# Kernel optimization log

Hardware: AMD Instinct MI355X
Metric: run time of the kernel (lower is better)

Reference implementation:

```python
import jax, jax.numpy as jnp
import numpy as np

N_NODES = 100000
N_EDGES = 1600000
IN_F, HID_F, OUT_F = 64, 64, 64


def setup_inputs() -> dict:
    key = jax.random.key(0)
    ks = jax.random.split(key, 9)
    return {
        "x": jax.random.normal(ks[0], (N_NODES, IN_F), dtype=jnp.float32),
        "src": jax.random.randint(ks[1], (N_EDGES,), 0, N_NODES, dtype=jnp.int64),
        "dst": jax.random.randint(ks[2], (N_EDGES,), 0, N_NODES, dtype=jnp.int64),
        "W_self1": jax.random.normal(ks[3], (IN_F, HID_F), dtype=jnp.float32) * (1.0 / np.sqrt(IN_F)),
        "W_neigh1": jax.random.normal(ks[4], (IN_F, HID_F), dtype=jnp.float32) * (1.0 / np.sqrt(IN_F)),
        "b1": jnp.zeros((HID_F,), dtype=jnp.float32),
        "W_self2": jax.random.normal(ks[5], (HID_F, OUT_F), dtype=jnp.float32) * (1.0 / np.sqrt(HID_F)),
        "W_neigh2": jax.random.normal(ks[6], (HID_F, OUT_F), dtype=jnp.float32) * (1.0 / np.sqrt(HID_F)),
        "b2": jnp.zeros((OUT_F,), dtype=jnp.float32),
    }


def reference(x, src, dst, W_self1, W_neigh1, b1, W_self2, W_neigh2, b2):
    N = x.shape[0]
    # in-degree per destination node; zero-in-degree nodes get zero aggregate (DGL semantics)
    deg = jax.ops.segment_sum(jnp.ones(dst.shape, dtype=x.dtype), dst, num_segments=N)
    inv_deg = jnp.where(deg > 0, 1.0 / jnp.maximum(deg, 1.0), 0.0)[:, None]  # [N,1]

    def sage_conv(h, W_s, W_n, b):
        # mean over in-neighbors: gather src feats, segment-sum at dst, normalize
        agg = jax.ops.segment_sum(h[src], dst, num_segments=N) * inv_deg  # [N,F]
        return h @ W_s + agg @ W_n + b

    h = jax.nn.relu(sage_conv(x, W_self1, W_neigh1, b1))
    return sage_conv(h, W_self2, W_neigh2, b2)
```

## Files before the change

### kernel.cpp

```cpp
#include <hip/hip_runtime.h>

#define N_NODES 100000
#define N_EDGES 1600000
#define NBKT 196
#define BKT_SHIFT 9
#define BKT_MASK 511

typedef __attribute__((ext_vector_type(8))) short short8;
typedef __attribute__((ext_vector_type(4))) float float4v;

__device__ __forceinline__ unsigned short f2bf(float f) {
  unsigned u = __float_as_uint(f);
  return (unsigned short)((u + 0x7fffu + ((u >> 16) & 1u)) >> 16);
}
__device__ __forceinline__ float bflo(unsigned d) { return __uint_as_float(d << 16); }
__device__ __forceinline__ float bfhi(unsigned d) { return __uint_as_float(d & 0xffff0000u); }


__global__ void kA_count(const int* __restrict__ dst, int* __restrict__ blkCnt) {
  __shared__ int hist[NBKT];
  for (int t = threadIdx.x; t < NBKT; t += 256) hist[t] = 0;
  __syncthreads();
  const int chunk = (N_EDGES + gridDim.x - 1) / gridDim.x;
  const int e0 = blockIdx.x * chunk;
  const int e1 = min(e0 + chunk, N_EDGES);
  for (int e = e0 + threadIdx.x; e < e1; e += 256)
    atomicAdd(&hist[dst[e] >> BKT_SHIFT], 1);
  __syncthreads();
  for (int t = threadIdx.x; t < NBKT; t += 256)
    blkCnt[t * 256 + blockIdx.x] = hist[t];
}

__global__ void kA_scan1(int* __restrict__ blkCnt, int* __restrict__ bktTot) {
  const int b = blockIdx.x;
  const int tid = threadIdx.x, lane = tid & 63, w = tid >> 6;
  int v = blkCnt[b * 256 + tid];
  int inc = v;
  #pragma unroll
  for (int d = 1; d < 64; d <<= 1) { int y = __shfl_up(inc, d); if (lane >= d) inc += y; }
  __shared__ int wtot[4];
  if (lane == 63) wtot[w] = inc;
  __syncthreads();
  int base = 0;
  for (int j = 0; j < w; j++) base += wtot[j];
  blkCnt[b * 256 + tid] = base + inc - v;
  if (tid == 255) bktTot[b] = base + inc;
}

__global__ void kA_scan2(const int* __restrict__ bktTot, int* __restrict__ bktStart) {
  int lane = threadIdx.x;
  int running = 0;
  for (int base = 0; base < NBKT; base += 64) {
    int i = base + lane;
    int v = (i < NBKT) ? bktTot[i] : 0;
    int inc = v;
    #pragma unroll
    for (int d = 1; d < 64; d <<= 1) { int y = __shfl_up(inc, d); if (lane >= d) inc += y; }
    if (i < NBKT) bktStart[i] = running + inc - v;
    running += __shfl(inc, 63);
  }
}

__global__ void kA_scatter(const int* __restrict__ src, const int* __restrict__ dst,
                           const int* __restrict__ blkCnt, const int* __restrict__ bktStart,
                           int* __restrict__ binned) {
  __shared__ int curb[NBKT];
  for (int t = threadIdx.x; t < NBKT; t += 256)
    curb[t] = bktStart[t] + blkCnt[t * 256 + blockIdx.x];
  __syncthreads();
  const int chunk = (N_EDGES + gridDim.x - 1) / gridDim.x;
  const int e0 = blockIdx.x * chunk;
  const int e1 = min(e0 + chunk, N_EDGES);
  for (int e = e0 + threadIdx.x; e < e1; e += 256) {
    int d = dst[e];
    int s = src[e];
    int b = d >> BKT_SHIFT;
    int p = atomicAdd(&curb[b], 1);
    binned[p] = s | ((d & BKT_MASK) << 17);
  }
}


__global__ void k_sort(const int* __restrict__ binned, const int* __restrict__ bktStart,
                       const int* __restrict__ bktTot,
                       int* __restrict__ off, int* __restrict__ esrc) {
  const int b = blockIdx.x;
  const int tid = threadIdx.x, lane = tid & 63, w = tid >> 6;
  __shared__ int cnt[512];
  __shared__ int pos[512];
  cnt[tid] = 0; cnt[tid + 256] = 0;
  __syncthreads();
  const int s0 = bktStart[b], ne = bktTot[b];
  for (int i = tid; i < ne; i += 256)
    atomicAdd(&cnt[binned[s0 + i] >> 17], 1);
  __syncthreads();
  int c0 = cnt[2 * tid], c1 = cnt[2 * tid + 1];
  int v = c0 + c1;
  int inc = v;
  #pragma unroll
  for (int d = 1; d < 64; d <<= 1) { int y = __shfl_up(inc, d); if (lane >= d) inc += y; }
  __shared__ int wtot[4];
  if (lane == 63) wtot[w] = inc;
  __syncthreads();
  int base = s0;
  for (int j = 0; j < w; j++) base += wtot[j];
  int ex = base + inc - v;
  pos[2 * tid] = ex;
  pos[2 * tid + 1] = ex + c0;
  int n0 = (b << BKT_SHIFT) + 2 * tid;
  if (n0 < N_NODES)     off[n0] = ex;
  if (n0 + 1 < N_NODES) off[n0 + 1] = ex + c0;
  if (b == NBKT - 1 && tid == 0) off[N_NODES] = N_EDGES;
  __syncthreads();
  for (int i = tid; i < ne; i += 256) {
    int pe = binned[s0 + i];
    int p = atomicAdd(&pos[pe >> 17], 1);
    esrc[p] = pe & 0x1FFFF;
  }
}


__global__ void k_cvt(const float* __restrict__ in, unsigned short* __restrict__ outb) {
  int i = blockIdx.x * blockDim.x + threadIdx.x;
  const int n4 = (N_NODES * 64) / 4;
  if (i < n4) {
    float4 v = ((const float4*)in)[i];
    unsigned d0 = ((unsigned)f2bf(v.y) << 16) | f2bf(v.x);
    unsigned d1 = ((unsigned)f2bf(v.w) << 16) | f2bf(v.z);
    ((uint2*)outb)[i] = make_uint2(d0, d1);
  }
}


__global__ void k_wprep(const float* __restrict__ W0, const float* __restrict__ W1,
                        const float* __restrict__ W2, const float* __restrict__ W3,
                        unsigned short* __restrict__ F) {
  const float* W = (blockIdx.x == 0) ? W0 : (blockIdx.x == 1) ? W1
                 : (blockIdx.x == 2) ? W2 : W3;
  unsigned short* out = F + blockIdx.x * 4096;
  int lane = threadIdx.x;
  int col = lane & 15, kr = lane >> 4;
  #pragma unroll
  for (int kc = 0; kc < 2; kc++)
    #pragma unroll
    for (int nt = 0; nt < 4; nt++) {
      unsigned d[4];
      #pragma unroll
      for (int jj = 0; jj < 4; jj++) {
        float w0 = W[(kc * 32 + kr * 8 + 2 * jj)     * 64 + nt * 16 + col];
        float w1 = W[(kc * 32 + kr * 8 + 2 * jj + 1) * 64 + nt * 16 + col];
        d[jj] = ((unsigned)f2bf(w1) << 16) | f2bf(w0);
      }
      uint4* p = (uint4*)(out + ((kc * 4 + nt) * 64 + lane) * 8);
      *p = make_uint4(d[0], d[1], d[2], d[3]);
    }
}


__global__ void k_agg(const unsigned short* __restrict__ featb,
                      const int* __restrict__ off, const int* __restrict__ esrc,
                      unsigned short* __restrict__ aggb) {
  const int lane = threadIdx.x & 63;
  const int r = lane >> 3;
  const int c = lane & 7;
  const int wid = (blockIdx.x * blockDim.x + threadIdx.x) >> 6;
  const int nw  = (gridDim.x * blockDim.x) >> 6;

  for (int n = wid; n < N_NODES; n += nw) {
    const int o0 = off[n], o1 = off[n + 1];
    float acc[8];
    #pragma unroll
    for (int j = 0; j < 8; j++) acc[j] = 0.f;

    int i = o0;
    for (; i + 16 <= o1; i += 16) {
      int sA = esrc[i + r];
      int sB = esrc[i + 8 + r];
      uint4 vA = *(const uint4*)(featb + sA * 64 + c * 8);
      uint4 vB = *(const uint4*)(featb + sB * 64 + c * 8);
      acc[0] += bflo(vA.x); acc[1] += bfhi(vA.x);
      acc[2] += bflo(vA.y); acc[3] += bfhi(vA.y);
      acc[4] += bflo(vA.z); acc[5] += bfhi(vA.z);
      acc[6] += bflo(vA.w); acc[7] += bfhi(vA.w);
      acc[0] += bflo(vB.x); acc[1] += bfhi(vB.x);
      acc[2] += bflo(vB.y); acc[3] += bfhi(vB.y);
      acc[4] += bflo(vB.z); acc[5] += bfhi(vB.z);
      acc[6] += bflo(vB.w); acc[7] += bfhi(vB.w);
    }
    if (i + 8 <= o1) {
      int s = esrc[i + r];
      uint4 v = *(const uint4*)(featb + s * 64 + c * 8);
      acc[0] += bflo(v.x); acc[1] += bfhi(v.x);
      acc[2] += bflo(v.y); acc[3] += bfhi(v.y);
      acc[4] += bflo(v.z); acc[5] += bfhi(v.z);
      acc[6] += bflo(v.w); acc[7] += bfhi(v.w);
      i += 8;
    }
    if (i < o1) {
      int e = i + r;
      if (e < o1) {
        int s = esrc[e];
        uint4 v = *(const uint4*)(featb + s * 64 + c * 8);
        acc[0] += bflo(v.x); acc[1] += bfhi(v.x);
        acc[2] += bflo(v.y); acc[3] += bfhi(v.y);
        acc[4] += bflo(v.z); acc[5] += bfhi(v.z);
        acc[6] += bflo(v.w); acc[7] += bfhi(v.w);
      }
    }
    #pragma unroll
    for (int m = 8; m <= 32; m <<= 1)
      #pragma unroll
      for (int j = 0; j < 8; j++) acc[j] += __shfl_xor(acc[j], m);

    const int dg = o1 - o0;
    const float inv = (dg > 0) ? (1.0f / (float)dg) : 0.f;
    if (r == 0) {
      unsigned d0 = ((unsigned)f2bf(acc[1] * inv) << 16) | f2bf(acc[0] * inv);
      unsigned d1 = ((unsigned)f2bf(acc[3] * inv) << 16) | f2bf(acc[2] * inv);
      unsigned d2 = ((unsigned)f2bf(acc[5] * inv) << 16) | f2bf(acc[4] * inv);
      unsigned d3 = ((unsigned)f2bf(acc[7] * inv) << 16) | f2bf(acc[6] * inv);
      *(uint4*)(aggb + n * 64 + c * 8) = make_uint4(d0, d1, d2, d3);
    }
  }
}


template <bool RELU, bool OUT_BF>
__global__ void k_xform(const unsigned short* __restrict__ selfb,
                        const unsigned short* __restrict__ aggb,
                        const unsigned short* __restrict__ wfS,
                        const unsigned short* __restrict__ wfN,
                        const float* __restrict__ bias,
                        float* __restrict__ outf, unsigned short* __restrict__ outb) {
  const int lane = threadIdx.x & 63;
  const int col = lane & 15, rr = lane >> 4;
  const int wid = (blockIdx.x * blockDim.x + threadIdx.x) >> 6;
  const int nw  = (gridDim.x * blockDim.x) >> 6;

  short8 bs[2][4], bn[2][4];
  #pragma unroll
  for (int kc = 0; kc < 2; kc++)
    #pragma unroll
    for (int nt = 0; nt < 4; nt++) {
      bs[kc][nt] = *(const short8*)(wfS + ((kc * 4 + nt) * 64 + lane) * 8);
      bn[kc][nt] = *(const short8*)(wfN + ((kc * 4 + nt) * 64 + lane) * 8);
    }
  float bv[4];
  #pragma unroll
  for (int nt = 0; nt < 4; nt++) bv[nt] = bias[nt * 16 + col];

  const int NT = N_NODES / 16;
  for (int t = wid; t < NT; t += nw) {
    const int m = t * 16 + col;
    short8 as0 = *(const short8*)(selfb + m * 64 + rr * 8);
    short8 as1 = *(const short8*)(selfb + m * 64 + 32 + rr * 8);
    short8 aa0 = *(const short8*)(aggb + m * 64 + rr * 8);
    short8 aa1 = *(const short8*)(aggb + m * 64 + 32 + rr * 8);
    #pragma unroll
    for (int nt = 0; nt < 4; nt++) {
      float4v cfr = {bv[nt], bv[nt], bv[nt], bv[nt]};
      cfr = __builtin_amdgcn_mfma_f32_16x16x32_bf16(as0, bs[0][nt], cfr, 0, 0, 0);
      cfr = __builtin_amdgcn_mfma_f32_16x16x32_bf16(as1, bs[1][nt], cfr, 0, 0, 0);
      cfr = __builtin_amdgcn_mfma_f32_16x16x32_bf16(aa0, bn[0][nt], cfr, 0, 0, 0);
      cfr = __builtin_amdgcn_mfma_f32_16x16x32_bf16(aa1, bn[1][nt], cfr, 0, 0, 0);
      #pragma unroll
      for (int r2 = 0; r2 < 4; r2++) {
        int row = t * 16 + rr * 4 + r2;
        float v = cfr[r2];
        if (RELU) v = fmaxf(v, 0.f);
        if (OUT_BF) outb[row * 64 + nt * 16 + col] = f2bf(v);
        else        outf[row * 64 + nt * 16 + col] = v;
      }
    }
  }
}


extern "C" void kernel_launch(void* const* d_in, const int* in_sizes, int n_in,
                              void* d_out, int out_size, void* d_ws, size_t ws_size,
                              hipStream_t stream) {
  const float* x   = (const float*)d_in[0];
  const int*   src = (const int*)d_in[1];
  const int*   dst = (const int*)d_in[2];
  const float* Ws1 = (const float*)d_in[3];
  const float* Wn1 = (const float*)d_in[4];
  const float* b1  = (const float*)d_in[5];
  const float* Ws2 = (const float*)d_in[6];
  const float* Wn2 = (const float*)d_in[7];
  const float* b2  = (const float*)d_in[8];

  char* ws = (char*)d_ws;
  int*            blkCnt   = (int*)(ws + 0);
  int*            bktTot   = (int*)(ws + 262144);
  int*            bktStart = (int*)(ws + 266240);
  unsigned short* wf       = (unsigned short*)(ws + 270336);
  int*            binned   = (int*)(ws + 303104);
  int*            off      = (int*)(ws + 6703104);
  int*            esrc     = (int*)(ws + 7103488);
  unsigned short* xbf      = (unsigned short*)(ws + 13503488);
  unsigned short* hbf      = (unsigned short*)(ws + 26303488);
  unsigned short* agg1     = (unsigned short*)(ws + 39103488);
  unsigned short* agg2     = (unsigned short*)(ws + 51903488);

  kA_count<<<256, 256, 0, stream>>>(dst, blkCnt);
  kA_scan1<<<NBKT, 256, 0, stream>>>(blkCnt, bktTot);
  kA_scan2<<<1, 64, 0, stream>>>(bktTot, bktStart);
  kA_scatter<<<256, 256, 0, stream>>>(src, dst, blkCnt, bktStart, binned);
  k_sort<<<NBKT, 256, 0, stream>>>(binned, bktStart, bktTot, off, esrc);

  k_cvt<<<(N_NODES * 16 + 255) / 256, 256, 0, stream>>>(x, xbf);
  k_wprep<<<4, 64, 0, stream>>>(Ws1, Wn1, Ws2, Wn2, wf);

  k_agg<<<2048, 256, 0, stream>>>(xbf, off, esrc, agg1);
  k_xform<true, true><<<1024, 256, 0, stream>>>(xbf, agg1, wf + 0 * 4096, wf + 1 * 4096,
                                                b1, nullptr, hbf);
  k_agg<<<2048, 256, 0, stream>>>(hbf, off, esrc, agg2);
  k_xform<false, false><<<1024, 256, 0, stream>>>(hbf, agg2, wf + 2 * 4096, wf + 3 * 4096,
                                                  b2, (float*)d_out, nullptr);
}
```

Before: 244.1 us.

## Fuse neighbor aggregation with MFMA transform per layer and merge prep kernels

Each layer now runs one kernel: every wavefront aggregates 16 destination nodes into a swizzled LDS tile and feeds it straight into the bf16 MFMA transform, with weights staged in shared memory. This removes the intermediate aggregate buffers and their global write and read-back, plus two launches. The x conversion and weight repacking are merged into a single prep kernel, and the per-bucket sort uses 512 threads with one node per thread. The risk is that fewer wavefronts are in flight (1563 blocks, and each wave handles 16 serial nodes), which could lower the memory-level parallelism of the gather.

```diff
diff --git a/kernel.cpp b/kernel.cpp
--- a/kernel.cpp
+++ b/kernel.cpp
@@ -81,38 +81,36 @@
 }
 
 
-__global__ void k_sort(const int* __restrict__ binned, const int* __restrict__ bktStart,
-                       const int* __restrict__ bktTot,
-                       int* __restrict__ off, int* __restrict__ esrc) {
+__global__ __launch_bounds__(512)
+void k_sort(const int* __restrict__ binned, const int* __restrict__ bktStart,
+            const int* __restrict__ bktTot,
+            int* __restrict__ off, int* __restrict__ esrc) {
   const int b = blockIdx.x;
   const int tid = threadIdx.x, lane = tid & 63, w = tid >> 6;
   __shared__ int cnt[512];
   __shared__ int pos[512];
-  cnt[tid] = 0; cnt[tid + 256] = 0;
+  cnt[tid] = 0;
   __syncthreads();
   const int s0 = bktStart[b], ne = bktTot[b];
-  for (int i = tid; i < ne; i += 256)
+  for (int i = tid; i < ne; i += 512)
     atomicAdd(&cnt[binned[s0 + i] >> 17], 1);
   __syncthreads();
-  int c0 = cnt[2 * tid], c1 = cnt[2 * tid + 1];
-  int v = c0 + c1;
+  int v = cnt[tid];
   int inc = v;
   #pragma unroll
   for (int d = 1; d < 64; d <<= 1) { int y = __shfl_up(inc, d); if (lane >= d) inc += y; }
-  __shared__ int wtot[4];
+  __shared__ int wtot[8];
   if (lane == 63) wtot[w] = inc;
   __syncthreads();
   int base = s0;
   for (int j = 0; j < w; j++) base += wtot[j];
   int ex = base + inc - v;
-  pos[2 * tid] = ex;
-  pos[2 * tid + 1] = ex + c0;
-  int n0 = (b << BKT_SHIFT) + 2 * tid;
-  if (n0 < N_NODES)     off[n0] = ex;
-  if (n0 + 1 < N_NODES) off[n0 + 1] = ex + c0;
+  pos[tid] = ex;
+  int n0 = (b << BKT_SHIFT) + tid;
+  if (n0 < N_NODES) off[n0] = ex;
   if (b == NBKT - 1 && tid == 0) off[N_NODES] = N_EDGES;
   __syncthreads();
-  for (int i = tid; i < ne; i += 256) {
+  for (int i = tid; i < ne; i += 512) {
     int pe = binned[s0 + i];
     int p = atomicAdd(&pos[pe >> 17], 1);
     esrc[p] = pe & 0x1FFFF;
@@ -120,24 +118,26 @@
 }
 
 
-__global__ void k_cvt(const float* __restrict__ in, unsigned short* __restrict__ outb) {
-  int i = blockIdx.x * blockDim.x + threadIdx.x;
-  const int n4 = (N_NODES * 64) / 4;
-  if (i < n4) {
-    float4 v = ((const float4*)in)[i];
-    unsigned d0 = ((unsigned)f2bf(v.y) << 16) | f2bf(v.x);
-    unsigned d1 = ((unsigned)f2bf(v.w) << 16) | f2bf(v.z);
-    ((uint2*)outb)[i] = make_uint2(d0, d1);
-  }
-}
-
-
-__global__ void k_wprep(const float* __restrict__ W0, const float* __restrict__ W1,
-                        const float* __restrict__ W2, const float* __restrict__ W3,
-                        unsigned short* __restrict__ F) {
-  const float* W = (blockIdx.x == 0) ? W0 : (blockIdx.x == 1) ? W1
-                 : (blockIdx.x == 2) ? W2 : W3;
-  unsigned short* out = F + blockIdx.x * 4096;
+__global__ void k_prep(const float* __restrict__ in, unsigned short* __restrict__ outb,
+                       const float* __restrict__ W0, const float* __restrict__ W1,
+                       const float* __restrict__ W2, const float* __restrict__ W3,
+                       unsigned short* __restrict__ F) {
+  const int NC = (N_NODES * 16 + 255) / 256;
+  if (blockIdx.x < NC) {
+    int i = blockIdx.x * 256 + threadIdx.x;
+    const int n4 = (N_NODES * 64) / 4;
+    if (i < n4) {
+      float4 v = ((const float4*)in)[i];
+      unsigned d0 = ((unsigned)f2bf(v.y) << 16) | f2bf(v.x);
+      unsigned d1 = ((unsigned)f2bf(v.w) << 16) | f2bf(v.z);
+      ((uint2*)outb)[i] = make_uint2(d0, d1);
+    }
+    return;
+  }
+  if (threadIdx.x >= 64) return;
+  const int q = blockIdx.x - NC;
+  const float* W = (q == 0) ? W0 : (q == 1) ? W1 : (q == 2) ? W2 : W3;
+  unsigned short* out = F + q * 4096;
   int lane = threadIdx.x;
   int col = lane & 15, kr = lane >> 4;
   #pragma unroll
@@ -157,112 +157,116 @@
 }
 
 
-__global__ void k_agg(const unsigned short* __restrict__ featb,
-                      const int* __restrict__ off, const int* __restrict__ esrc,
-                      unsigned short* __restrict__ aggb) {
-  const int lane = threadIdx.x & 63;
-  const int r = lane >> 3;
-  const int c = lane & 7;
-  const int wid = (blockIdx.x * blockDim.x + threadIdx.x) >> 6;
-  const int nw  = (gridDim.x * blockDim.x) >> 6;
-
-  for (int n = wid; n < N_NODES; n += nw) {
-    const int o0 = off[n], o1 = off[n + 1];
-    float acc[8];
-    #pragma unroll
-    for (int j = 0; j < 8; j++) acc[j] = 0.f;
-
-    int i = o0;
-    for (; i + 16 <= o1; i += 16) {
-      int sA = esrc[i + r];
-      int sB = esrc[i + 8 + r];
-      uint4 vA = *(const uint4*)(featb + sA * 64 + c * 8);
-      uint4 vB = *(const uint4*)(featb + sB * 64 + c * 8);
-      acc[0] += bflo(vA.x); acc[1] += bfhi(vA.x);
-      acc[2] += bflo(vA.y); acc[3] += bfhi(vA.y);
-      acc[4] += bflo(vA.z); acc[5] += bfhi(vA.z);
-      acc[6] += bflo(vA.w); acc[7] += bfhi(vA.w);
-      acc[0] += bflo(vB.x); acc[1] += bfhi(vB.x);
-      acc[2] += bflo(vB.y); acc[3] += bfhi(vB.y);
-      acc[4] += bflo(vB.z); acc[5] += bfhi(vB.z);
-      acc[6] += bflo(vB.w); acc[7] += bfhi(vB.w);
-    }
-    if (i + 8 <= o1) {
-      int s = esrc[i + r];
-      uint4 v = *(const uint4*)(featb + s * 64 + c * 8);
-      acc[0] += bflo(v.x); acc[1] += bfhi(v.x);
-      acc[2] += bflo(v.y); acc[3] += bfhi(v.y);
-      acc[4] += bflo(v.z); acc[5] += bfhi(v.z);
-      acc[6] += bflo(v.w); acc[7] += bfhi(v.w);
-      i += 8;
-    }
-    if (i < o1) {
-      int e = i + r;
-      if (e < o1) {
-        int s = esrc[e];
+template <bool RELU, bool OUT_BF>
+__global__ __launch_bounds__(256)
+void k_layerf(const unsigned short* __restrict__ featb,
+              const int* __restrict__ off, const int* __restrict__ esrc,
+              const unsigned short* __restrict__ wfS,
+              const unsigned short* __restrict__ wfN,
+              const float* __restrict__ bias,
+              float* __restrict__ outf, unsigned short* __restrict__ outb) {
+  __shared__ unsigned short wlds[8192];
+  __shared__ unsigned short atile[4][1024];
+
+  const int tid = threadIdx.x;
+  {
+    const uint4* gs = (const uint4*)wfS;
+    const uint4* gn = (const uint4*)wfN;
+    uint4* l = (uint4*)wlds;
+    for (int i = tid; i < 512; i += 256) { l[i] = gs[i]; l[512 + i] = gn[i]; }
+  }
+  __syncthreads();
+
+  const int lane = tid & 63;
+  const int wib  = tid >> 6;
+  const int r = lane >> 3, c = lane & 7;
+  const int col = lane & 15, rr = lane >> 4;
+  const int wid = (blockIdx.x << 2) | wib;
+  const int nw  = gridDim.x << 2;
+
+  float bv[4];
+  #pragma unroll
+  for (int nt = 0; nt < 4; nt++) bv[nt] = bias[nt * 16 + col];
+
+  unsigned short* at = atile[wib];
+  const int NT = N_NODES / 16;
+
+  for (int t = wid; t < NT; t += nw) {
+    for (int m = 0; m < 16; m++) {
+      const int n = t * 16 + m;
+      const int o0 = off[n], o1 = off[n + 1];
+      float acc[8];
+      #pragma unroll
+      for (int j = 0; j < 8; j++) acc[j] = 0.f;
+
+      int i = o0;
+      for (; i + 16 <= o1; i += 16) {
+        int sA = esrc[i + r];
+        int sB = esrc[i + 8 + r];
+        uint4 vA = *(const uint4*)(featb + sA * 64 + c * 8);
+        uint4 vB = *(const uint4*)(featb + sB * 64 + c * 8);
+        acc[0] += bflo(vA.x); acc[1] += bfhi(vA.x);
+        acc[2] += bflo(vA.y); acc[3] += bfhi(vA.y);
+        acc[4] += bflo(vA.z); acc[5] += bfhi(vA.z);
+        acc[6] += bflo(vA.w); acc[7] += bfhi(vA.w);
+        acc[0] += bflo(vB.x); acc[1] += bfhi(vB.x);
+        acc[2] += bflo(vB.y); acc[3] += bfhi(vB.y);
+        acc[4] += bflo(vB.z); acc[5] += bfhi(vB.z);
+        acc[6] += bflo(vB.w); acc[7] += bfhi(vB.w);
+      }
+      if (i + 8 <= o1) {
+        int s = esrc[i + r];
         uint4 v = *(const uint4*)(featb + s * 64 + c * 8);
         acc[0] += bflo(v.x); acc[1] += bfhi(v.x);
         acc[2] += bflo(v.y); acc[3] += bfhi(v.y);
         acc[4] += bflo(v.z); acc[5] += bfhi(v.z);
         acc[6] += bflo(v.w); acc[7] += bfhi(v.w);
+        i += 8;
+      }
+      if (i < o1) {
+        int e = i + r;
+        if (e < o1) {
+          int s = esrc[e];
+          uint4 v = *(const uint4*)(featb + s * 64 + c * 8);
+          acc[0] += bflo(v.x); acc[1] += bfhi(v.x);
+          acc[2] += bflo(v.y); acc[3] += bfhi(v.y);
+          acc[4] += bflo(v.z); acc[5] += bfhi(v.z);
+          acc[6] += bflo(v.w); acc[7] += bfhi(v.w);
+        }
+      }
+      #pragma unroll
+      for (int mm = 8; mm <= 32; mm <<= 1)
+        #pragma unroll
+        for (int j = 0; j < 8; j++) acc[j] += __shfl_xor(acc[j], mm);
+
+      const int dg = o1 - o0;
+      const float inv = (dg > 0) ? (1.0f / (float)dg) : 0.f;
+      if (r == 0) {
+        unsigned d0 = ((unsigned)f2bf(acc[1] * inv) << 16) | f2bf(acc[0] * inv);
+        unsigned d1 = ((unsigned)f2bf(acc[3] * inv) << 16) | f2bf(acc[2] * inv);
+        unsigned d2 = ((unsigned)f2bf(acc[5] * inv) << 16) | f2bf(acc[4] * inv);
+        unsigned d3 = ((unsigned)f2bf(acc[7] * inv) << 16) | f2bf(acc[6] * inv);
+        uint4* p = (uint4*)(at + (c >> 2) * 512 + (c & 3) * 128 + (((m + 2 * c) & 15) * 8));
+        *p = make_uint4(d0, d1, d2, d3);
       }
     }
-    #pragma unroll
-    for (int m = 8; m <= 32; m <<= 1)
-      #pragma unroll
-      for (int j = 0; j < 8; j++) acc[j] += __shfl_xor(acc[j], m);
-
-    const int dg = o1 - o0;
-    const float inv = (dg > 0) ? (1.0f / (float)dg) : 0.f;
-    if (r == 0) {
-      unsigned d0 = ((unsigned)f2bf(acc[1] * inv) << 16) | f2bf(acc[0] * inv);
-      unsigned d1 = ((unsigned)f2bf(acc[3] * inv) << 16) | f2bf(acc[2] * inv);
-      unsigned d2 = ((unsigned)f2bf(acc[5] * inv) << 16) | f2bf(acc[4] * inv);
-      unsigned d3 = ((unsigned)f2bf(acc[7] * inv) << 16) | f2bf(acc[6] * inv);
-      *(uint4*)(aggb + n * 64 + c * 8) = make_uint4(d0, d1, d2, d3);
-    }
-  }
-}
-
-
-template <bool RELU, bool OUT_BF>
-__global__ void k_xform(const unsigned short* __restrict__ selfb,
-                        const unsigned short* __restrict__ aggb,
-                        const unsigned short* __restrict__ wfS,
-                        const unsigned short* __restrict__ wfN,
-                        const float* __restrict__ bias,
-                        float* __restrict__ outf, unsigned short* __restrict__ outb) {
-  const int lane = threadIdx.x & 63;
-  const int col = lane & 15, rr = lane >> 4;
-  const int wid = (blockIdx.x * blockDim.x + threadIdx.x) >> 6;
-  const int nw  = (gridDim.x * blockDim.x) >> 6;
-
-  short8 bs[2][4], bn[2][4];
-  #pragma unroll
-  for (int kc = 0; kc < 2; kc++)
+
+    const int mrow = t * 16 + col;
+    short8 as0 = *(const short8*)(featb + mrow * 64 + rr * 8);
+    short8 as1 = *(const short8*)(featb + mrow * 64 + 32 + rr * 8);
+    short8 aa0 = *(const short8*)(at + rr * 128 + (((col + 2 * rr) & 15) * 8));
+    short8 aa1 = *(const short8*)(at + 512 + rr * 128 + (((col + 2 * rr + 8) & 15) * 8));
     #pragma unroll
     for (int nt = 0; nt < 4; nt++) {
-      bs[kc][nt] = *(const short8*)(wfS + ((kc * 4 + nt) * 64 + lane) * 8);
-      bn[kc][nt] = *(const short8*)(wfN + ((kc * 4 + nt) * 64 + lane) * 8);
-    }
-  float bv[4];
-  #pragma unroll
-  for (int nt = 0; nt < 4; nt++) bv[nt] = bias[nt * 16 + col];
-
-  const int NT = N_NODES / 16;
-  for (int t = wid; t < NT; t += nw) {
-    const int m = t * 16 + col;
-    short8 as0 = *(const short8*)(selfb + m * 64 + rr * 8);
-    short8 as1 = *(const short8*)(selfb + m * 64 + 32 + rr * 8);
-    short8 aa0 = *(const short8*)(aggb + m * 64 + rr * 8);
-    short8 aa1 = *(const short8*)(aggb + m * 64 + 32 + rr * 8);
-    #pragma unroll
-    for (int nt = 0; nt < 4; nt++) {
+      short8 b0 = *(const short8*)(wlds + ((0 * 4 + nt) * 64 + lane) * 8);
+      short8 b1 = *(const short8*)(wlds + ((1 * 4 + nt) * 64 + lane) * 8);
+      short8 c0 = *(const short8*)(wlds + 4096 + ((0 * 4 + nt) * 64 + lane) * 8);
+      short8 c1 = *(const short8*)(wlds + 4096 + ((1 * 4 + nt) * 64 + lane) * 8);
       float4v cfr = {bv[nt], bv[nt], bv[nt], bv[nt]};
-      cfr = __builtin_amdgcn_mfma_f32_16x16x32_bf16(as0, bs[0][nt], cfr, 0, 0, 0);
-      cfr = __builtin_amdgcn_mfma_f32_16x16x32_bf16(as1, bs[1][nt], cfr, 0, 0, 0);
-      cfr = __builtin_amdgcn_mfma_f32_16x16x32_bf16(aa0, bn[0][nt], cfr, 0, 0, 0);
-      cfr = __builtin_amdgcn_mfma_f32_16x16x32_bf16(aa1, bn[1][nt], cfr, 0, 0, 0);
+      cfr = __builtin_amdgcn_mfma_f32_16x16x32_bf16(as0, b0, cfr, 0, 0, 0);
+      cfr = __builtin_amdgcn_mfma_f32_16x16x32_bf16(as1, b1, cfr, 0, 0, 0);
+      cfr = __builtin_amdgcn_mfma_f32_16x16x32_bf16(aa0, c0, cfr, 0, 0, 0);
+      cfr = __builtin_amdgcn_mfma_f32_16x16x32_bf16(aa1, c1, cfr, 0, 0, 0);
       #pragma unroll
       for (int r2 = 0; r2 < 4; r2++) {
         int row = t * 16 + rr * 4 + r2;
@@ -299,22 +303,17 @@
   int*            esrc     = (int*)(ws + 7103488);
   unsigned short* xbf      = (unsigned short*)(ws + 13503488);
   unsigned short* hbf      = (unsigned short*)(ws + 26303488);
-  unsigned short* agg1     = (unsigned short*)(ws + 39103488);
-  unsigned short* agg2     = (unsigned short*)(ws + 51903488);
 
   kA_count<<<256, 256, 0, stream>>>(dst, blkCnt);
   kA_scan1<<<NBKT, 256, 0, stream>>>(blkCnt, bktTot);
   kA_scan2<<<1, 64, 0, stream>>>(bktTot, bktStart);
   kA_scatter<<<256, 256, 0, stream>>>(src, dst, blkCnt, bktStart, binned);
-  k_sort<<<NBKT, 256, 0, stream>>>(binned, bktStart, bktTot, off, esrc);
-
-  k_cvt<<<(N_NODES * 16 + 255) / 256, 256, 0, stream>>>(x, xbf);
-  k_wprep<<<4, 64, 0, stream>>>(Ws1, Wn1, Ws2, Wn2, wf);
-
-  k_agg<<<2048, 256, 0, stream>>>(xbf, off, esrc, agg1);
-  k_xform<true, true><<<1024, 256, 0, stream>>>(xbf, agg1, wf + 0 * 4096, wf + 1 * 4096,
-                                                b1, nullptr, hbf);
-  k_agg<<<2048, 256, 0, stream>>>(hbf, off, esrc, agg2);
-  k_xform<false, false><<<1024, 256, 0, stream>>>(hbf, agg2, wf + 2 * 4096, wf + 3 * 4096,
-                                                  b2, (float*)d_out, nullptr);
-}
+  k_sort<<<NBKT, 512, 0, stream>>>(binned, bktStart, bktTot, off, esrc);
+
+  k_prep<<<6254, 256, 0, stream>>>(x, xbf, Ws1, Wn1, Ws2, Wn2, wf);
+
+  k_layerf<true,  true ><<<1563, 256, 0, stream>>>(xbf, off, esrc, wf + 0 * 4096,
+                                                   wf + 1 * 4096, b1, nullptr, hbf);
+  k_layerf<false, false><<<1563, 256, 0, stream>>>(hbf, off, esrc, wf + 2 * 4096,
+                                                   wf + 3 * 4096, b2, (float*)d_out, nullptr);
+}
```

Result: slower. 326.5 us (+33.8%).
